# Kernel tuning notes

Hardware: AMD Instinct MI355X
Metric: run time of the kernel (lower is better)

The kernel has to match this reference:

```python
import jax, jax.numpy as jnp
import numpy as np

B, N, IN_DIM, OUT_DIM, HEADS = 32, 10, 65536, 64, 8
D = OUT_DIM // HEADS  # = 8; torch.matmul only typechecks because D == HEADS


def setup_inputs() -> dict:
    key = jax.random.key(0)
    k1, k2, k3 = jax.random.split(key, 3)
    x = jax.random.normal(k1, (B, N, IN_DIM), dtype=jnp.float32)
    adj = jax.random.uniform(k2, (B, N, N), dtype=jnp.float32)
    # nn.Linear(in_dim, out_dim, bias=False) weight has shape (out_dim, in_dim)
    W = jax.random.normal(k3, (OUT_DIM, IN_DIM), dtype=jnp.float32) / np.float32(np.sqrt(IN_DIM))
    return {"x": x, "adj": adj, "W": W}


def reference(x, adj, W):
    b, n, _ = x.shape
    # W(x): (B, N, out_dim) -> view (B, N, heads, D)
    xt = (x @ W.T).reshape(b, n, HEADS, D)
    # torch.matmul(x_transformed, adj_expanded) with adj_expanded[b,n,k,m] = adj[b,n,m]
    # => result[b,n,h,m] = sum_k xt[b,n,h,k] * adj[b,n,m]
    result = jnp.einsum('bnhk,bnm->bnhm', xt, adj)
    result = result.reshape(32, 10, -1)  # hardcoded in the original module
    return jax.nn.relu(result)
```

## Files before the change

kernel.cpp:

```cpp
#include <hip/hip_runtime.h>
#include <hip/hip_bf16.h>

#define NN 10
#define IN_DIM 65536
#define HEADS 8
#define DD 8
#define ROWS 320
#define MTILES 20
#define KGRPS 512
#define KB_PER_GRP 4
#define KFLOATS 128
#define PAIRS (ROWS*HEADS)
#define LROW 136

typedef __attribute__((ext_vector_type(8))) short bf16x8;
typedef __attribute__((ext_vector_type(4))) float f32x4;
typedef unsigned short u16;

static __device__ __forceinline__ short f2bf(float f) {
    __hip_bfloat16 h = __float2bfloat16(f);
    return *reinterpret_cast<short*>(&h);
}
static __device__ __forceinline__ u16 f2bfu(float f) {
    __hip_bfloat16 h = __float2bfloat16(f);
    return *reinterpret_cast<u16*>(&h);
}
static __device__ __forceinline__ ushort4 cvt4(float4 v) {
    ushort4 o; o.x=f2bfu(v.x); o.y=f2bfu(v.y); o.z=f2bfu(v.z); o.w=f2bfu(v.w);
    return o;
}

struct XR { float4 r0,r1,r2,r3,r4,r5,r6,r7; };

static __device__ __forceinline__ void load_stage(XR& d, const float* __restrict__ x,
                                                  int kgrp, int s, int t) {
    const float* base = x + (size_t)kgrp * KFLOATS + (t & 31) * 4
                          + (size_t)(64 * s + (t >> 5)) * IN_DIM;
    d.r0 = *(const float4*)(base + (size_t)( 0) * IN_DIM);
    d.r1 = *(const float4*)(base + (size_t)( 8) * IN_DIM);
    d.r2 = *(const float4*)(base + (size_t)(16) * IN_DIM);
    d.r3 = *(const float4*)(base + (size_t)(24) * IN_DIM);
    d.r4 = *(const float4*)(base + (size_t)(32) * IN_DIM);
    d.r5 = *(const float4*)(base + (size_t)(40) * IN_DIM);
    d.r6 = *(const float4*)(base + (size_t)(48) * IN_DIM);
    d.r7 = *(const float4*)(base + (size_t)(56) * IN_DIM);
}

static __device__ __forceinline__ void write_stage(const XR& d, u16* __restrict__ buf, int t) {
    u16* p = buf + (size_t)(t >> 5) * LROW + (t & 31) * 4;
    *(ushort4*)(p + (size_t)( 0) * LROW) = cvt4(d.r0);
    *(ushort4*)(p + (size_t)( 8) * LROW) = cvt4(d.r1);
    *(ushort4*)(p + (size_t)(16) * LROW) = cvt4(d.r2);
    *(ushort4*)(p + (size_t)(24) * LROW) = cvt4(d.r3);
    *(ushort4*)(p + (size_t)(32) * LROW) = cvt4(d.r4);
    *(ushort4*)(p + (size_t)(40) * LROW) = cvt4(d.r5);
    *(ushort4*)(p + (size_t)(48) * LROW) = cvt4(d.r6);
    *(ushort4*)(p + (size_t)(56) * LROW) = cvt4(d.r7);
}

__global__ __launch_bounds__(256, 2) void gemv_fused_kernel(const float* __restrict__ x,
                                                            const float* __restrict__ W,
                                                            float* __restrict__ partials) {
    const int kgrp = blockIdx.x;
    const int t    = threadIdx.x;
    const int lane = t & 63;
    const int wave = t >> 6;

    __shared__ bf16x8 lds_b[KB_PER_GRP][64];
    __shared__ __align__(16) u16 xbuf[2][64][LROW];

    XR A, B;
    load_stage(A, x, kgrp, 0, t);

    {
        const int kbl  = t >> 6;
        const int head = lane & 15;
        const int kq   = lane >> 4;
        bf16x8 o = {0,0,0,0,0,0,0,0};
        if (head < HEADS) {
            float s0=0,s1=0,s2=0,s3=0,s4=0,s5=0,s6=0,s7=0;
            const float* wbase = W + (size_t)(head * DD) * IN_DIM
                               + kgrp * KFLOATS + kbl * 32 + kq * 8;
#pragma unroll
            for (int d = 0; d < DD; ++d) {
                const float4* p = (const float4*)(wbase + (size_t)d * IN_DIM);
                float4 lo = p[0], hi = p[1];
                s0 += lo.x; s1 += lo.y; s2 += lo.z; s3 += lo.w;
                s4 += hi.x; s5 += hi.y; s6 += hi.z; s7 += hi.w;
            }
            o[0]=f2bf(s0); o[1]=f2bf(s1); o[2]=f2bf(s2); o[3]=f2bf(s3);
            o[4]=f2bf(s4); o[5]=f2bf(s5); o[6]=f2bf(s6); o[7]=f2bf(s7);
        }
        lds_b[kbl][lane] = o;
    }
    __syncthreads();

    const bf16x8 b0 = lds_b[0][lane];
    const bf16x8 b1 = lds_b[1][lane];
    const bf16x8 b2 = lds_b[2][lane];
    const bf16x8 b3 = lds_b[3][lane];

    write_stage(A, &xbuf[0][0][0], t);
    load_stage(B, x, kgrp, 1, t);
    __syncthreads();

    const int head = lane & 15;
    const int r0   = (lane >> 4) * 4;
    const int kq   = lane >> 4;
    float* pbase = partials + (size_t)kgrp * PAIRS;
    const u16* rowp = &xbuf[0][0][0] + (size_t)(wave * 16 + (lane & 15)) * LROW + kq * 8;
    const size_t bufstride = (size_t)64 * LROW;

#define COMPUTE_STAGE(BUFIDX, MT)                                              \
    {                                                                          \
        const bf16x8* q = (const bf16x8*)(rowp + (BUFIDX) * bufstride);        \
        f32x4 acc = {0.f,0.f,0.f,0.f};                                         \
        acc = __builtin_amdgcn_mfma_f32_16x16x32_bf16(q[0],  b0, acc, 0,0,0);  \
        acc = __builtin_amdgcn_mfma_f32_16x16x32_bf16(q[4],  b1, acc, 0,0,0);  \
        acc = __builtin_amdgcn_mfma_f32_16x16x32_bf16(q[8],  b2, acc, 0,0,0);  \
        acc = __builtin_amdgcn_mfma_f32_16x16x32_bf16(q[12], b3, acc, 0,0,0);  \
        if (head < HEADS) {                                                    \
            _Pragma("unroll")                                                  \
            for (int j = 0; j < 4; ++j)                                        \
                pbase[(size_t)((MT)*16 + r0 + j) * HEADS + head] = acc[j];     \
        }                                                                      \
    }

    load_stage(A, x, kgrp, 2, t);
    COMPUTE_STAGE(0, wave);
    __syncthreads();
    write_stage(B, &xbuf[1][0][0], t);
    __syncthreads();

    load_stage(B, x, kgrp, 3, t);
    COMPUTE_STAGE(1, 4 + wave);
    __syncthreads();
    write_stage(A, &xbuf[0][0][0], t);
    __syncthreads();

    load_stage(A, x, kgrp, 4, t);
    COMPUTE_STAGE(0, 8 + wave);
    __syncthreads();
    write_stage(B, &xbuf[1][0][0], t);
    __syncthreads();

    COMPUTE_STAGE(1, 12 + wave);
    __syncthreads();
    write_stage(A, &xbuf[0][0][0], t);
    __syncthreads();

    COMPUTE_STAGE(0, 16 + wave);
#undef COMPUTE_STAGE
}

__global__ __launch_bounds__(256) void finalize_kernel(const float* __restrict__ partials,
                                                       const float* __restrict__ adj,
                                                       float* __restrict__ out) {
    const int b  = blockIdx.x;
    const int t  = threadIdx.x;
    const int pr = t & 15;
    const int gs = t >> 4;
    const int pair = b * 16 + pr;

    float s = 0.f;
    const float* p = partials + (size_t)gs * 32 * PAIRS + pair;
#pragma unroll 8
    for (int g = 0; g < 32; ++g)
        s += p[(size_t)g * PAIRS];

    __shared__ float red[16][16];
    red[gs][pr] = s;
    __syncthreads();

    if (t < 16) {
        float tot = 0.f;
#pragma unroll
        for (int i = 0; i < 16; ++i) tot += red[i][t];
        const int pair2 = b * 16 + t;
        const int bn = pair2 >> 3;
        const int h  = pair2 & 7;
        const float* a = adj + bn * NN;
        float* o = out + bn * (HEADS * NN) + h * NN;
#pragma unroll
        for (int m = 0; m < NN; ++m) {
            float v = tot * a[m];
            o[m] = v > 0.f ? v : 0.f;
        }
    }
}

extern "C" void kernel_launch(void* const* d_in, const int* in_sizes, int n_in,
                              void* d_out, int out_size, void* d_ws, size_t ws_size,
                              hipStream_t stream) {
    const float* x   = (const float*)d_in[0];
    const float* adj = (const float*)d_in[1];
    const float* W   = (const float*)d_in[2];
    float* out = (float*)d_out;

    float* partials = (float*)d_ws;

    gemv_fused_kernel<<<KGRPS, 256, 0, stream>>>(x, W, partials);
    finalize_kernel<<<160, 256, 0, stream>>>(partials, adj, out);
}
```

Measured before the change: 24.94 us.

## Store partials as bf16 head-major and prefetch second x stage earlier

The per-block partial sums are now written as bf16 in a head-major layout with one packed 8-byte store per lane, replacing four scattered fp32 stores. The finalize kernel reads and widens them, so partial traffic is halved. The second x stage load is also issued before the W reduction to overlap more global latency. This adds bf16 rounding error to every partial before the 512-way reduction and raises register pressure from keeping two stages in flight.

```diff
diff --git a/kernel.cpp b/kernel.cpp
--- a/kernel.cpp
+++ b/kernel.cpp
@@ -24,6 +24,10 @@
 static __device__ __forceinline__ u16 f2bfu(float f) {
     __hip_bfloat16 h = __float2bfloat16(f);
     return *reinterpret_cast<u16*>(&h);
+}
+static __device__ __forceinline__ float bf2f(u16 u) {
+    unsigned int v = ((unsigned int)u) << 16;
+    return *reinterpret_cast<float*>(&v);
 }
 static __device__ __forceinline__ ushort4 cvt4(float4 v) {
     ushort4 o; o.x=f2bfu(v.x); o.y=f2bfu(v.y); o.z=f2bfu(v.z); o.w=f2bfu(v.w);
@@ -60,7 +64,7 @@
 
 __global__ __launch_bounds__(256, 2) void gemv_fused_kernel(const float* __restrict__ x,
                                                             const float* __restrict__ W,
-                                                            float* __restrict__ partials) {
+                                                            u16* __restrict__ partials) {
     const int kgrp = blockIdx.x;
     const int t    = threadIdx.x;
     const int lane = t & 63;
@@ -71,6 +75,7 @@
 
     XR A, B;
     load_stage(A, x, kgrp, 0, t);
+    load_stage(B, x, kgrp, 1, t);
 
     {
         const int kbl  = t >> 6;
@@ -101,13 +106,12 @@
     const bf16x8 b3 = lds_b[3][lane];
 
     write_stage(A, &xbuf[0][0][0], t);
-    load_stage(B, x, kgrp, 1, t);
     __syncthreads();
 
     const int head = lane & 15;
     const int r0   = (lane >> 4) * 4;
     const int kq   = lane >> 4;
-    float* pbase = partials + (size_t)kgrp * PAIRS;
+    u16* pbase = partials + (size_t)kgrp * PAIRS;
     const u16* rowp = &xbuf[0][0][0] + (size_t)(wave * 16 + (lane & 15)) * LROW + kq * 8;
     const size_t bufstride = (size_t)64 * LROW;
 
@@ -120,9 +124,8 @@
         acc = __builtin_amdgcn_mfma_f32_16x16x32_bf16(q[8],  b2, acc, 0,0,0);  \
         acc = __builtin_amdgcn_mfma_f32_16x16x32_bf16(q[12], b3, acc, 0,0,0);  \
         if (head < HEADS) {                                                    \
-            _Pragma("unroll")                                                  \
-            for (int j = 0; j < 4; ++j)                                        \
-                pbase[(size_t)((MT)*16 + r0 + j) * HEADS + head] = acc[j];     \
+            float4 av; av.x=acc[0]; av.y=acc[1]; av.z=acc[2]; av.w=acc[3];     \
+            *(ushort4*)&pbase[(size_t)head * ROWS + (MT)*16 + r0] = cvt4(av);  \
         }                                                                      \
     }
 
@@ -153,7 +156,7 @@
 #undef COMPUTE_STAGE
 }
 
-__global__ __launch_bounds__(256) void finalize_kernel(const float* __restrict__ partials,
+__global__ __launch_bounds__(256) void finalize_kernel(const u16* __restrict__ partials,
                                                        const float* __restrict__ adj,
                                                        float* __restrict__ out) {
     const int b  = blockIdx.x;
@@ -161,12 +164,14 @@
     const int pr = t & 15;
     const int gs = t >> 4;
     const int pair = b * 16 + pr;
+    const int bn = pair >> 3;
+    const int h  = pair & 7;
 
     float s = 0.f;
-    const float* p = partials + (size_t)gs * 32 * PAIRS + pair;
+    const u16* p = partials + (size_t)gs * 32 * PAIRS + (size_t)h * ROWS + bn;
 #pragma unroll 8
     for (int g = 0; g < 32; ++g)
-        s += p[(size_t)g * PAIRS];
+        s += bf2f(p[(size_t)g * PAIRS]);
 
     __shared__ float red[16][16];
     red[gs][pr] = s;
@@ -177,10 +182,10 @@
 #pragma unroll
         for (int i = 0; i < 16; ++i) tot += red[i][t];
         const int pair2 = b * 16 + t;
-        const int bn = pair2 >> 3;
-        const int h  = pair2 & 7;
-        const float* a = adj + bn * NN;
-        float* o = out + bn * (HEADS * NN) + h * NN;
+        const int bn2 = pair2 >> 3;
+        const int h2  = pair2 & 7;
+        const float* a = adj + bn2 * NN;
+        float* o = out + bn2 * (HEADS * NN) + h2 * NN;
 #pragma unroll
         for (int m = 0; m < NN; ++m) {
             float v = tot * a[m];
@@ -197,7 +202,7 @@
     const float* W   = (const float*)d_in[2];
     float* out = (float*)d_out;
 
-    float* partials = (float*)d_ws;
+    u16* partials = (u16*)d_ws;
 
     gemv_fused_kernel<<<KGRPS, 256, 0, stream>>>(x, W, partials);
     finalize_kernel<<<160, 256, 0, stream>>>(partials, adj, out);
```

Result: slower. 27.48 us (+10.2%).
